# Kernel tuning notes

Hardware: AMD Instinct MI355X
Metric: run time of the kernel (lower is better)

The kernel has to match this reference:

```python
import jax, jax.numpy as jnp
import numpy as np

N1 = 4096
N2 = 4096


def _encoder(x, w1, b1, w2, b2, w3, b3):
    # fc1 -> fc2 -> fc3 -> relu (relu only after fc3, matching the torch code)
    h = x @ w1.T + b1
    h = h @ w2.T + b2
    h = h @ w3.T + b3
    return jax.nn.relu(h)


def _self_attention(x, adj, alpha, W):
    # tmp_i = sum_j [adj_ij==1] * alpha_ij * W * x_j ; tmp_i /= deg_i ; tmp_i += x_i (only if deg_i != 0)
    a = (adj == 1).astype(x.dtype)          # [N, N]
    deg = a.sum(axis=1)                     # [N]
    agg = (a * alpha) @ x                   # [N, 64] masked weighted aggregation
    agg = agg * W[0, 0]
    safe_deg = jnp.maximum(deg, 1.0)
    out = agg / safe_deg[:, None] + x       # residual
    return jnp.where((deg != 0.0)[:, None], out, jnp.zeros_like(out))


def setup_inputs() -> dict:
    key = jax.random.key(0)
    ks = jax.random.split(key, 20)
    s = 0.02  # weight scale to keep activations sane through the 4096->256->128->64 MLP
    inp = {
        "x1": jax.random.normal(ks[0], (N1, N1), jnp.float32),
        "x2": jax.random.normal(ks[1], (N2, N2), jnp.float32),
        "adj1": jax.random.randint(ks[2], (N1, N1), 0, 2, jnp.int32),
        "adj2": jax.random.randint(ks[3], (N2, N2), 0, 2, jnp.int32),
        "e1_w1": jax.random.normal(ks[4], (256, N1), jnp.float32) * s,
        "e1_b1": jnp.zeros((256,), jnp.float32),
        "e1_w2": jax.random.normal(ks[5], (128, 256), jnp.float32) * s,
        "e1_b2": jnp.zeros((128,), jnp.float32),
        "e1_w3": jax.random.normal(ks[6], (64, 128), jnp.float32) * s,
        "e1_b3": jnp.zeros((64,), jnp.float32),
        "e2_w1": jax.random.normal(ks[7], (256, N2), jnp.float32) * s,
        "e2_b1": jnp.zeros((256,), jnp.float32),
        "e2_w2": jax.random.normal(ks[8], (128, 256), jnp.float32) * s,
        "e2_b2": jnp.zeros((128,), jnp.float32),
        "e2_w3": jax.random.normal(ks[9], (64, 128), jnp.float32) * s,
        "e2_b3": jnp.zeros((64,), jnp.float32),
        "W": jax.random.normal(ks[10], (1, 1), jnp.float32),
        "alpha1": jax.random.normal(ks[11], (N1, N1), jnp.float32),
        "clf_w": jax.random.normal(ks[12], (2, (N1 + N2) * 64), jnp.float32) * s,
        "clf_b": jnp.zeros((2,), jnp.float32),
    }
    return inp


def reference(x1, x2, adj1, adj2,
              e1_w1, e1_b1, e1_w2, e1_b2, e1_w3, e1_b3,
              e2_w1, e2_b1, e2_w2, e2_b2, e2_w3, e2_b3,
              W, alpha1, clf_w, clf_b):
    h1 = _encoder(x1, e1_w1, e1_b1, e1_w2, e1_b2, e1_w3, e1_b3)  # [N1, 64]
    h2 = _encoder(x2, e2_w1, e2_b1, e2_w2, e2_b2, e2_w3, e2_b3)  # [N2, 64]
    # NOTE: original torch code uses self.alpha1 for BOTH graphs (alpha2 is unused)
    new1 = _self_attention(h1, adj1, alpha1, W)
    new2 = _self_attention(h2, adj2, alpha1[:N2, :N2], W)
    feat = jnp.concatenate([new1, new2], axis=0).reshape(1, -1)  # [1, (N1+N2)*64]
    return feat @ clf_w.T + clf_b  # [1, 2]
```

## Files before the change

kernel.cpp:

```cpp
#include <hip/hip_runtime.h>
#include <hip/hip_bf16.h>
#include <stdint.h>

#define N 4096

typedef __attribute__((ext_vector_type(4))) float f32x4;
typedef __attribute__((ext_vector_type(8))) short s16x8;

__device__ inline unsigned short f2bf(float f) {
    unsigned int u = __float_as_uint(f);
    u += 0x7fffu + ((u >> 16) & 1u);
    return (unsigned short)(u >> 16);
}
__device__ inline float bf2f(unsigned short h) {
    return __uint_as_float(((unsigned int)h) << 16);
}

__global__ void k0a(const float* __restrict__ w2a, const float* __restrict__ w3a,
                    const float* __restrict__ b1a, const float* __restrict__ b2a, const float* __restrict__ b3a,
                    const float* __restrict__ w2b, const float* __restrict__ w3b,
                    const float* __restrict__ b1b, const float* __restrict__ b2b, const float* __restrict__ b3b,
                    float* __restrict__ T, float* __restrict__ beff) {
    const int g  = blockIdx.x >> 5;
    const int nb = blockIdx.x & 31;
    const float* w2 = g ? w2b : w2a;
    const float* w3 = g ? w3b : w3a;
    const int c  = threadIdx.x;
    const int n0 = nb * 2;
    float a0 = 0.f, a1 = 0.f;
#pragma unroll 8
    for (int r = 0; r < 128; ++r) {
        float w = w2[r * 256 + c];
        a0 += w3[n0 * 128 + r] * w;
        a1 += w3[n0 * 128 + 128 + r] * w;
    }
    float* Tg = T + g * 64 * 256;
    Tg[n0 * 256 + c]       = a0;
    Tg[(n0 + 1) * 256 + c] = a1;

    if (nb == 0) {
        __shared__ float ps[256];
        __shared__ float u[128];
        const float* b1 = g ? b1b : b1a;
        const float* b2 = g ? b2b : b2a;
        const float* b3 = g ? b3b : b3a;
        {
            const int r = threadIdx.x >> 1, half = threadIdx.x & 1;
            float s = 0.f;
#pragma unroll 8
            for (int cc = 0; cc < 128; ++cc) s += w2[r * 256 + half * 128 + cc] * b1[half * 128 + cc];
            ps[threadIdx.x] = s;
        }
        __syncthreads();
        if (threadIdx.x < 128)
            u[threadIdx.x] = ps[2 * threadIdx.x] + ps[2 * threadIdx.x + 1] + b2[threadIdx.x];
        __syncthreads();
        {
            const int n = threadIdx.x >> 2, qr = threadIdx.x & 3;
            float s = 0.f;
#pragma unroll
            for (int r = 0; r < 32; ++r) s += w3[n * 128 + qr * 32 + r] * u[qr * 32 + r];
            ps[threadIdx.x] = s;
        }
        __syncthreads();
        if (threadIdx.x < 64)
            beff[g * 64 + threadIdx.x] = ps[4 * threadIdx.x] + ps[4 * threadIdx.x + 1]
                                       + ps[4 * threadIdx.x + 2] + ps[4 * threadIdx.x + 3] + b3[threadIdx.x];
    }
}

__global__ __launch_bounds__(256) void k0b(const float* __restrict__ w1a, const float* __restrict__ w1b,
                                           const float* __restrict__ T,
                                           unsigned short* __restrict__ Wfrag) {
    const int b  = blockIdx.x;
    const int g = b >> 8, n4 = (b >> 4) & 15, kchunk = b & 15;
    const float* w1 = g ? w1b : w1a;
    const int kx = kchunk * 256 + threadIdx.x;
    const float* Tg = T + (size_t)(g * 64 + n4 * 4) * 256;
    float acc[4] = {0.f, 0.f, 0.f, 0.f};
#pragma unroll 8
    for (int r = 0; r < 256; ++r) {
        float w = w1[(size_t)r * N + kx];
#pragma unroll
        for (int j = 0; j < 4; ++j) acc[j] += Tg[j * 256 + r] * w;
    }
    const int kc = kx >> 6, cc = (kx >> 5) & 1, q = (kx >> 3) & 3, ko = kx & 7;
#pragma unroll
    for (int j = 0; j < 4; ++j) {
        const int n = n4 * 4 + j;
        const int ng = n >> 4, l15 = n & 15;
        const int lane = q * 16 + l15;
        const unsigned short hi = f2bf(acc[j]);
        const unsigned short lo = f2bf(acc[j] - bf2f(hi));
        const size_t unit = ((((size_t)g * 64 + kc) * 4 + ng) * 2 + cc) * 2;
        Wfrag[unit * 512 + lane * 8 + ko]       = hi;
        Wfrag[(unit + 1) * 512 + lane * 8 + ko] = lo;
    }
}

__global__ __launch_bounds__(512, 4) void k1(const float* __restrict__ x1, const float* __restrict__ x2,
                                             const unsigned short* __restrict__ Wfrag,
                                             const float* __restrict__ beff,
                                             float* __restrict__ hf, unsigned short* __restrict__ hfrag) {
    const int b  = blockIdx.x;
    const int g  = b & 1;
    const int i0 = (b >> 1) * 16;
    const float* x = g ? x2 : x1;

    const int t = threadIdx.x;
    const int lane = t & 63, kg = t >> 6;
    const int q = lane >> 4, l15 = lane & 15;

    __shared__ float accs[8][4][64][4];
    __shared__ unsigned short htile[64][16];

    f32x4 acc[4];
#pragma unroll
    for (int ng = 0; ng < 4; ++ng) acc[ng] = (f32x4){0.f, 0.f, 0.f, 0.f};

    const float* xrow = x + (size_t)(i0 + l15) * N;
    for (int kk = 0; kk < 8; ++kk) {
        const int kc = kg * 8 + kk;
#pragma unroll
        for (int c = 0; c < 2; ++c) {
            const int ka = kc * 64 + c * 32 + q * 8;
            float4 a0 = *(const float4*)&xrow[ka];
            float4 a1 = *(const float4*)&xrow[ka + 4];
            s16x8 bh[4], bl[4];
#pragma unroll
            for (int ng = 0; ng < 4; ++ng) {
                const size_t unit = ((((size_t)g * 64 + kc) * 4 + ng) * 2 + c) * 2;
                bh[ng] = *(const s16x8*)&Wfrag[unit * 512 + lane * 8];
                bl[ng] = *(const s16x8*)&Wfrag[(unit + 1) * 512 + lane * 8];
            }
            float xv[8] = {a0.x, a0.y, a0.z, a0.w, a1.x, a1.y, a1.z, a1.w};
            s16x8 ah, al;
#pragma unroll
            for (int j = 0; j < 8; ++j) {
                unsigned short h = f2bf(xv[j]);
                ah[j] = (short)h;
                al[j] = (short)f2bf(xv[j] - bf2f(h));
            }
#pragma unroll
            for (int ng = 0; ng < 4; ++ng) {
                acc[ng] = __builtin_amdgcn_mfma_f32_16x16x32_bf16(al, bh[ng], acc[ng], 0, 0, 0);
                acc[ng] = __builtin_amdgcn_mfma_f32_16x16x32_bf16(ah, bl[ng], acc[ng], 0, 0, 0);
                acc[ng] = __builtin_amdgcn_mfma_f32_16x16x32_bf16(ah, bh[ng], acc[ng], 0, 0, 0);
            }
        }
    }
#pragma unroll
    for (int ng = 0; ng < 4; ++ng)
#pragma unroll
        for (int r = 0; r < 4; ++r) accs[kg][ng][lane][r] = acc[ng][r];
    __syncthreads();

    {
        const int ng = kg & 3, rh = kg >> 2;
        const int n = ng * 16 + l15;
        const float be = beff[g * 64 + n];
#pragma unroll
        for (int rr = 0; rr < 2; ++rr) {
            const int r = rh * 2 + rr;
            float s = 0.f;
#pragma unroll
            for (int k8 = 0; k8 < 8; ++k8) s += accs[k8][ng][lane][r];
            float v = fmaxf(s + be, 0.f);
            const int il = q * 4 + r;
            hf[(size_t)(g * N + i0 + il) * 64 + n] = v;
            htile[n][il] = f2bf(v);
        }
    }
    __syncthreads();

    if (t < 128) {
        const int ng2 = t >> 5, jh = (t >> 4) & 1, l = t & 15;
        uint4 v = *(const uint4*)&htile[ng2 * 16 + l][jh * 8];
        const int jc = i0 >> 6, c = (i0 >> 5) & 1, q0 = (i0 >> 3) & 3;
        const size_t unit = (((size_t)g * 4 + ng2) * 64 + jc) * 2 + c;
        *(uint4*)&hfrag[unit * 512 + (size_t)(q0 + jh) * 128 + l * 8] = v;
    }
}

__global__ __launch_bounds__(512, 2) void k2(const int* __restrict__ adj1, const int* __restrict__ adj2,
                                             const float* __restrict__ alpha,
                                             const unsigned short* __restrict__ hfrag,
                                             float* __restrict__ pagg, float* __restrict__ pdeg) {
    const int b  = blockIdx.x;
    const int ks = (b >> 1) & 3;
    const int i0 = ((((b >> 3) << 1) | (b & 1))) << 4;
    const int t = threadIdx.x;
    const int lane = t & 63, kg = t >> 6;
    const int q = lane >> 4, l15 = lane & 15;

    __shared__ __align__(16) unsigned short am[2][2][16][256];
    __shared__ float degp[2][16][32];
    float (*accs)[4][64][4] = reinterpret_cast<float (*)[4][64][4]>(&am[0][0][0][0]);

    f32x4 acc1[4], acc2[4];
#pragma unroll
    for (int ng = 0; ng < 4; ++ng) {
        acc1[ng] = (f32x4){0.f, 0.f, 0.f, 0.f};
        acc2[ng] = (f32x4){0.f, 0.f, 0.f, 0.f};
    }
    int deg1 = 0, deg2 = 0;

    const int srow = t >> 5, scg = t & 31;
    const size_t sbase = (size_t)(i0 + srow) * N + (size_t)ks * 1024 + (size_t)scg * 8;
    char* const amb = (char*)&am[0][0][0][0];
    const int swoff = (srow * 512 + scg * 16) ^ ((srow & 7) << 4);
    const int rdoff = (l15 * 512 + kg * 64 + q * 16) ^ ((l15 & 7) << 4);

    float4 sa0, sa1; int4 sj10, sj11, sj20, sj21;

#define K2_ISSUE(S) do { \
        const float* ap = alpha + sbase + (S) * 256; \
        sa0 = *(const float4*)ap; sa1 = *(const float4*)(ap + 4); \
        const int* p1 = adj1 + sbase + (S) * 256; \
        sj10 = *(const int4*)p1; sj11 = *(const int4*)(p1 + 4); \
        const int* p2 = adj2 + sbase + (S) * 256; \
        sj20 = *(const int4*)p2; sj21 = *(const int4*)(p2 + 4); \
    } while (0)

#define K2_CONVSTORE(BUF) do { \
        float av[8] = {sa0.x, sa0.y, sa0.z, sa0.w, sa1.x, sa1.y, sa1.z, sa1.w}; \
        int m1[8] = {sj10.x == 1, sj10.y == 1, sj10.z == 1, sj10.w == 1, \
                     sj11.x == 1, sj11.y == 1, sj11.z == 1, sj11.w == 1}; \
        int m2[8] = {sj20.x == 1, sj20.y == 1, sj20.z == 1, sj20.w == 1, \
                     sj21.x == 1, sj21.y == 1, sj21.z == 1, sj21.w == 1}; \
        s16x8 w1v, w2v; \
        _Pragma("unroll") \
        for (int j = 0; j < 8; ++j) { \
            unsigned short bv = f2bf(av[j]); \
            w1v[j] = m1[j] ? (short)bv : (short)0; \
            w2v[j] = m2[j] ? (short)bv : (short)0; \
            deg1 += m1[j]; deg2 += m2[j]; \
        } \
        *(s16x8*)(amb + (BUF) * 16384 + swoff) = w1v; \
        *(s16x8*)(amb + (BUF) * 16384 + 8192 + swoff) = w2v; \
    } while (0)

#define K2_COMPUTE(S) do { \
        const int jc = ks * 16 + (S) * 4 + (kg >> 1), cph = kg & 1; \
        s16x8 ha1[4], ha2[4]; \
        _Pragma("unroll") \
        for (int ng = 0; ng < 4; ++ng) { \
            const size_t u1 = (((size_t)ng) * 64 + jc) * 2 + cph; \
            const size_t u2 = (((size_t)(4 + ng)) * 64 + jc) * 2 + cph; \
            ha1[ng] = *(const s16x8*)&hfrag[u1 * 512 + lane * 8]; \
            ha2[ng] = *(const s16x8*)&hfrag[u2 * 512 + lane * 8]; \
        } \
        s16x8 bfa = *(const s16x8*)(amb + ((S) & 1) * 16384 + rdoff); \
        s16x8 bfb = *(const s16x8*)(amb + ((S) & 1) * 16384 + 8192 + rdoff); \
        _Pragma("unroll") \
        for (int ng = 0; ng < 4; ++ng) { \
            acc1[ng] = __builtin_amdgcn_mfma_f32_16x16x32_bf16(ha1[ng], bfa, acc1[ng], 0, 0, 0); \
            acc2[ng] = __builtin_amdgcn_mfma_f32_16x16x32_bf16(ha2[ng], bfb, acc2[ng], 0, 0, 0); \
        } \
    } while (0)

    K2_ISSUE(0);
    K2_CONVSTORE(0);
    __syncthreads();
#pragma unroll
    for (int s = 0; s < 4; ++s) {
        if (s < 3) K2_ISSUE(s + 1);
        K2_COMPUTE(s);
        if (s < 3) K2_CONVSTORE((s + 1) & 1);
        __syncthreads();
    }

    degp[0][srow][scg] = (float)deg1;
    degp[1][srow][scg] = (float)deg2;
#pragma unroll
    for (int ng = 0; ng < 4; ++ng)
#pragma unroll
        for (int r = 0; r < 4; ++r) accs[kg][ng][lane][r] = acc1[ng][r];
    __syncthreads();
    if (t < 32) {
        const int gg = t >> 4, row = t & 15;
        float s = 0.f;
#pragma unroll
        for (int c2 = 0; c2 < 32; ++c2) s += degp[gg][row][c2];
        pdeg[(size_t)(gg * 4 + ks) * 4096 + i0 + row] = s;
    }

    {
        const int ng = kg & 3, rh = kg >> 2;
        const int i = i0 + l15;
#pragma unroll
        for (int rr = 0; rr < 2; ++rr) {
            const int r = rh * 2 + rr;
            float s = 0.f;
#pragma unroll
            for (int k8 = 0; k8 < 8; ++k8) s += accs[k8][ng][lane][r];
            const int n = ng * 16 + q * 4 + r;
            pagg[(((size_t)ks * 4096 + i) << 6) + n] = s;
        }
    }
    __syncthreads();
#pragma unroll
    for (int ng = 0; ng < 4; ++ng)
#pragma unroll
        for (int r = 0; r < 4; ++r) accs[kg][ng][lane][r] = acc2[ng][r];
    __syncthreads();
    {
        const int ng = kg & 3, rh = kg >> 2;
        const int i = i0 + l15;
#pragma unroll
        for (int rr = 0; rr < 2; ++rr) {
            const int r = rh * 2 + rr;
            float s = 0.f;
#pragma unroll
            for (int k8 = 0; k8 < 8; ++k8) s += accs[k8][ng][lane][r];
            const int n = ng * 16 + q * 4 + r;
            pagg[(((size_t)(4 + ks) * 4096 + i) << 6) + n] = s;
        }
    }
#undef K2_ISSUE
#undef K2_CONVSTORE
#undef K2_COMPUTE
}

__global__ __launch_bounds__(256) void k2b(const float* __restrict__ pagg, const float* __restrict__ pdeg,
                                           const float* __restrict__ hf, const float* __restrict__ Wp,
                                           float* __restrict__ outv) {
    const int idx = blockIdx.x * 256 + threadIdx.x;
    const int gi  = idx >> 4;
    const int nq  = idx & 15;
    const int g   = gi >> 12, i = gi & 4095;
    const float W00 = Wp[0];

    float dg = 0.f;
#pragma unroll
    for (int ks = 0; ks < 4; ++ks) dg += pdeg[(size_t)(g * 4 + ks) * 4096 + i];

    f32x4 s = (f32x4){0.f, 0.f, 0.f, 0.f};
#pragma unroll
    for (int ks = 0; ks < 4; ++ks) {
        const f32x4 p = *(const f32x4*)&pagg[(((size_t)(g * 4 + ks) * 4096 + i) << 6) + nq * 4];
        s += p;
    }
    const f32x4 hv = *(const f32x4*)&hf[((size_t)gi << 6) + nq * 4];
    const float dmax = fmaxf(dg, 1.f);
    f32x4 o;
#pragma unroll
    for (int j = 0; j < 4; ++j)
        o[j] = (dg != 0.f) ? (s[j] * W00 / dmax + hv[j]) : 0.f;
    *(f32x4*)&outv[((size_t)gi << 6) + nq * 4] = o;
}

__global__ __launch_bounds__(256) void k3a(const float* __restrict__ feat, const float* __restrict__ clfw,
                                           float* __restrict__ part) {
    const int t = threadIdx.x;
    const size_t idx = (size_t)blockIdx.x * 2048 + (size_t)t * 8;
    float4 a0 = *(const float4*)&feat[idx];
    float4 a1 = *(const float4*)&feat[idx + 4];
    float4 c0 = *(const float4*)&clfw[idx];
    float4 c1 = *(const float4*)&clfw[idx + 4];
    float4 d0 = *(const float4*)&clfw[524288 + idx];
    float4 d1 = *(const float4*)&clfw[524288 + idx + 4];
    float s0 = a0.x * c0.x + a0.y * c0.y + a0.z * c0.z + a0.w * c0.w
             + a1.x * c1.x + a1.y * c1.y + a1.z * c1.z + a1.w * c1.w;
    float s1 = a0.x * d0.x + a0.y * d0.y + a0.z * d0.z + a0.w * d0.w
             + a1.x * d1.x + a1.y * d1.y + a1.z * d1.z + a1.w * d1.w;
    __shared__ float r0[256], r1[256];
    r0[t] = s0; r1[t] = s1;
    __syncthreads();
    for (int s = 128; s > 0; s >>= 1) {
        if (t < s) { r0[t] += r0[t + s]; r1[t] += r1[t + s]; }
        __syncthreads();
    }
    if (t == 0) { part[blockIdx.x * 2] = r0[0]; part[blockIdx.x * 2 + 1] = r1[0]; }
}

__global__ void k3b(const float* __restrict__ part, const float* __restrict__ clfb,
                    float* __restrict__ outp) {
    const int t = threadIdx.x;
    __shared__ float r0[256], r1[256];
    r0[t] = part[t * 2]; r1[t] = part[t * 2 + 1];
    __syncthreads();
    for (int s = 128; s > 0; s >>= 1) {
        if (t < s) { r0[t] += r0[t + s]; r1[t] += r1[t + s]; }
        __syncthreads();
    }
    if (t == 0) { outp[0] = r0[0] + clfb[0]; outp[1] = r1[0] + clfb[1]; }
}

extern "C" void kernel_launch(void* const* d_in, const int* in_sizes, int n_in,
                              void* d_out, int out_size, void* d_ws, size_t ws_size,
                              hipStream_t stream) {
    const float* x1   = (const float*)d_in[0];
    const float* x2   = (const float*)d_in[1];
    const int*   adj1 = (const int*)d_in[2];
    const int*   adj2 = (const int*)d_in[3];
    const float* e1w1 = (const float*)d_in[4];
    const float* e1b1 = (const float*)d_in[5];
    const float* e1w2 = (const float*)d_in[6];
    const float* e1b2 = (const float*)d_in[7];
    const float* e1w3 = (const float*)d_in[8];
    const float* e1b3 = (const float*)d_in[9];
    const float* e2w1 = (const float*)d_in[10];
    const float* e2b1 = (const float*)d_in[11];
    const float* e2w2 = (const float*)d_in[12];
    const float* e2b2 = (const float*)d_in[13];
    const float* e2w3 = (const float*)d_in[14];
    const float* e2b3 = (const float*)d_in[15];
    const float* Wp   = (const float*)d_in[16];
    const float* alph = (const float*)d_in[17];
    const float* clfw = (const float*)d_in[18];
    const float* clfb = (const float*)d_in[19];

    char* wsb = (char*)d_ws;
    unsigned short* Wfrag = (unsigned short*)(wsb);
    float* newv = (float*)(wsb);
    unsigned short* hfrag = (unsigned short*)(wsb + (2u << 20));
    float* hf   = (float*)(wsb + (3u << 20));
    float* T    = (float*)(wsb + (5u << 20));
    float* beff = (float*)(wsb + (5u << 20) + (1u << 17));
    float* part = (float*)(wsb + (5u << 20) + (1u << 17) + 4096);
    float* pagg = (float*)(wsb + (6u << 20));
    float* pdeg = (float*)(wsb + (14u << 20));

    hipLaunchKernelGGL(k0a, dim3(64), dim3(256), 0, stream,
                       e1w2, e1w3, e1b1, e1b2, e1b3, e2w2, e2w3, e2b1, e2b2, e2b3, T, beff);
    hipLaunchKernelGGL(k0b, dim3(512), dim3(256), 0, stream, e1w1, e2w1, T, Wfrag);
    hipLaunchKernelGGL(k1, dim3(512), dim3(512), 0, stream, x1, x2, Wfrag, beff, hf, hfrag);
    hipLaunchKernelGGL(k2, dim3(1024), dim3(512), 0, stream, adj1, adj2, alph, hfrag, pagg, pdeg);
    hipLaunchKernelGGL(k2b, dim3(512), dim3(256), 0, stream, pagg, pdeg, hf, Wp, newv);
    hipLaunchKernelGGL(k3a, dim3(256), dim3(256), 0, stream, newv, clfw, part);
    hipLaunchKernelGGL(k3b, dim3(1), dim3(256), 0, stream, part, clfb, (float*)d_out);
}
```

Baseline: 395.0 us.

## Split k1 GEMM into 64-row tiles with split-K partials and separate reduce kernel

k1 now gives each block 64 rows and a quarter of K, so each Wfrag fragment loaded is reused across four row groups instead of one. Partial sums go to a workspace buffer, and a new k1b kernel sums them and applies bias and relu before writing hf and hfrag. The main loop is also unrolled with double-buffered register loads so the next x and W fragments are fetched while the MFMAs run. In exchange it adds an extra launch, a round trip of the partials through global memory, and higher register pressure (launch bounds lowered to 2 blocks).

```diff
diff --git a/kernel.cpp b/kernel.cpp
--- a/kernel.cpp
+++ b/kernel.cpp
@@ -98,79 +98,118 @@
     }
 }
 
-__global__ __launch_bounds__(512, 4) void k1(const float* __restrict__ x1, const float* __restrict__ x2,
+__global__ __launch_bounds__(512, 2) void k1(const float* __restrict__ x1, const float* __restrict__ x2,
                                              const unsigned short* __restrict__ Wfrag,
-                                             const float* __restrict__ beff,
-                                             float* __restrict__ hf, unsigned short* __restrict__ hfrag) {
+                                             float* __restrict__ ph) {
     const int b  = blockIdx.x;
-    const int g  = b & 1;
-    const int i0 = (b >> 1) * 16;
+    const int rt = b >> 2, ks = b & 3;
+    const int g  = rt >> 6;
+    const int rbase = (rt & 63) * 64;
     const float* x = g ? x2 : x1;
 
     const int t = threadIdx.x;
-    const int lane = t & 63, kg = t >> 6;
+    const int lane = t & 63, w = t >> 6;
+    const int rg = w & 3, kh = w >> 2;
     const int q = lane >> 4, l15 = lane & 15;
 
-    __shared__ float accs[8][4][64][4];
-    __shared__ unsigned short htile[64][16];
+    __shared__ float accs_h[4][4][64][4];
 
     f32x4 acc[4];
 #pragma unroll
     for (int ng = 0; ng < 4; ++ng) acc[ng] = (f32x4){0.f, 0.f, 0.f, 0.f};
 
-    const float* xrow = x + (size_t)(i0 + l15) * N;
-    for (int kk = 0; kk < 8; ++kk) {
-        const int kc = kg * 8 + kk;
-#pragma unroll
-        for (int c = 0; c < 2; ++c) {
-            const int ka = kc * 64 + c * 32 + q * 8;
-            float4 a0 = *(const float4*)&xrow[ka];
-            float4 a1 = *(const float4*)&xrow[ka + 4];
-            s16x8 bh[4], bl[4];
-#pragma unroll
-            for (int ng = 0; ng < 4; ++ng) {
-                const size_t unit = ((((size_t)g * 64 + kc) * 4 + ng) * 2 + c) * 2;
-                bh[ng] = *(const s16x8*)&Wfrag[unit * 512 + lane * 8];
-                bl[ng] = *(const s16x8*)&Wfrag[(unit + 1) * 512 + lane * 8];
-            }
-            float xv[8] = {a0.x, a0.y, a0.z, a0.w, a1.x, a1.y, a1.z, a1.w};
-            s16x8 ah, al;
-#pragma unroll
-            for (int j = 0; j < 8; ++j) {
-                unsigned short h = f2bf(xv[j]);
-                ah[j] = (short)h;
-                al[j] = (short)f2bf(xv[j] - bf2f(h));
-            }
-#pragma unroll
-            for (int ng = 0; ng < 4; ++ng) {
-                acc[ng] = __builtin_amdgcn_mfma_f32_16x16x32_bf16(al, bh[ng], acc[ng], 0, 0, 0);
-                acc[ng] = __builtin_amdgcn_mfma_f32_16x16x32_bf16(ah, bl[ng], acc[ng], 0, 0, 0);
-                acc[ng] = __builtin_amdgcn_mfma_f32_16x16x32_bf16(ah, bh[ng], acc[ng], 0, 0, 0);
+    const float* xrow = x + (size_t)(rbase + rg * 16 + l15) * N;
+    const int kcbase = ks * 16 + kh * 8;
+
+    float4 pa0, pa1, ra0, ra1;
+    s16x8 pbh[4], pbl[4], rbh[4], rbl[4];
+
+#define K1_LOAD(A0, A1, BH, BL, IT) do { \
+        const int kc_ = kcbase + ((IT) >> 1), c_ = (IT) & 1; \
+        const int ka_ = kc_ * 64 + c_ * 32 + q * 8; \
+        A0 = *(const float4*)&xrow[ka_]; \
+        A1 = *(const float4*)&xrow[ka_ + 4]; \
+        _Pragma("unroll") \
+        for (int ng = 0; ng < 4; ++ng) { \
+            const size_t unit = ((((size_t)g * 64 + kc_) * 4 + ng) * 2 + c_) * 2; \
+            BH[ng] = *(const s16x8*)&Wfrag[unit * 512 + lane * 8]; \
+            BL[ng] = *(const s16x8*)&Wfrag[(unit + 1) * 512 + lane * 8]; \
+        } \
+    } while (0)
+
+#define K1_COMP(A0, A1, BH, BL) do { \
+        float xv[8] = {A0.x, A0.y, A0.z, A0.w, A1.x, A1.y, A1.z, A1.w}; \
+        s16x8 ah, al; \
+        _Pragma("unroll") \
+        for (int j = 0; j < 8; ++j) { \
+            unsigned short hh = f2bf(xv[j]); \
+            ah[j] = (short)hh; \
+            al[j] = (short)f2bf(xv[j] - bf2f(hh)); \
+        } \
+        _Pragma("unroll") \
+        for (int ng = 0; ng < 4; ++ng) { \
+            acc[ng] = __builtin_amdgcn_mfma_f32_16x16x32_bf16(al, BH[ng], acc[ng], 0, 0, 0); \
+            acc[ng] = __builtin_amdgcn_mfma_f32_16x16x32_bf16(ah, BL[ng], acc[ng], 0, 0, 0); \
+            acc[ng] = __builtin_amdgcn_mfma_f32_16x16x32_bf16(ah, BH[ng], acc[ng], 0, 0, 0); \
+        } \
+    } while (0)
+
+    K1_LOAD(pa0, pa1, pbh, pbl, 0);
+#pragma unroll
+    for (int it2 = 0; it2 < 8; ++it2) {
+        K1_LOAD(ra0, ra1, rbh, rbl, 2 * it2 + 1);
+        K1_COMP(pa0, pa1, pbh, pbl);
+        if (it2 < 7) K1_LOAD(pa0, pa1, pbh, pbl, 2 * it2 + 2);
+        K1_COMP(ra0, ra1, rbh, rbl);
+    }
+#undef K1_LOAD
+#undef K1_COMP
+
+    if (kh == 1) {
+#pragma unroll
+        for (int ng = 0; ng < 4; ++ng)
+#pragma unroll
+            for (int r = 0; r < 4; ++r) accs_h[rg][ng][lane][r] = acc[ng][r];
+    }
+    __syncthreads();
+    if (kh == 0) {
+        const int girow = g * 4096 + rbase + rg * 16 + q * 4;
+#pragma unroll
+        for (int ng = 0; ng < 4; ++ng) {
+            const int n = ng * 16 + l15;
+#pragma unroll
+            for (int r = 0; r < 4; ++r) {
+                float s = acc[ng][r] + accs_h[rg][ng][lane][r];
+                ph[((size_t)ks * 8192 + girow + r) * 64 + n] = s;
             }
         }
     }
-#pragma unroll
-    for (int ng = 0; ng < 4; ++ng)
-#pragma unroll
-        for (int r = 0; r < 4; ++r) accs[kg][ng][lane][r] = acc[ng][r];
-    __syncthreads();
-
-    {
-        const int ng = kg & 3, rh = kg >> 2;
-        const int n = ng * 16 + l15;
-        const float be = beff[g * 64 + n];
-#pragma unroll
-        for (int rr = 0; rr < 2; ++rr) {
-            const int r = rh * 2 + rr;
-            float s = 0.f;
-#pragma unroll
-            for (int k8 = 0; k8 < 8; ++k8) s += accs[k8][ng][lane][r];
-            float v = fmaxf(s + be, 0.f);
-            const int il = q * 4 + r;
-            hf[(size_t)(g * N + i0 + il) * 64 + n] = v;
-            htile[n][il] = f2bf(v);
-        }
-    }
+}
+
+__global__ __launch_bounds__(256) void k1b(const float* __restrict__ ph, const float* __restrict__ beff,
+                                           float* __restrict__ hf, unsigned short* __restrict__ hfrag) {
+    const int b = blockIdx.x;
+    const int g = b & 1;
+    const int i0 = (b >> 1) * 16;
+    const int t = threadIdx.x;
+    const int il = t >> 4, nq = t & 15;
+    const int gi = g * 4096 + i0 + il;
+
+    __shared__ unsigned short htile[64][16];
+
+    f32x4 s = (f32x4){0.f, 0.f, 0.f, 0.f};
+#pragma unroll
+    for (int ks = 0; ks < 4; ++ks)
+        s += *(const f32x4*)&ph[((size_t)ks * 8192 + gi) * 64 + nq * 4];
+    f32x4 o;
+#pragma unroll
+    for (int j = 0; j < 4; ++j) {
+        const int n = nq * 4 + j;
+        float v = fmaxf(s[j] + beff[g * 64 + n], 0.f);
+        o[j] = v;
+        htile[n][il] = f2bf(v);
+    }
+    *(f32x4*)&hf[(size_t)gi * 64 + nq * 4] = o;
     __syncthreads();
 
     if (t < 128) {
@@ -420,12 +459,14 @@
     float* beff = (float*)(wsb + (5u << 20) + (1u << 17));
     float* part = (float*)(wsb + (5u << 20) + (1u << 17) + 4096);
     float* pagg = (float*)(wsb + (6u << 20));
+    float* ph   = (float*)(wsb + (6u << 20));
     float* pdeg = (float*)(wsb + (14u << 20));
 
     hipLaunchKernelGGL(k0a, dim3(64), dim3(256), 0, stream,
                        e1w2, e1w3, e1b1, e1b2, e1b3, e2w2, e2w3, e2b1, e2b2, e2b3, T, beff);
     hipLaunchKernelGGL(k0b, dim3(512), dim3(256), 0, stream, e1w1, e2w1, T, Wfrag);
-    hipLaunchKernelGGL(k1, dim3(512), dim3(512), 0, stream, x1, x2, Wfrag, beff, hf, hfrag);
+    hipLaunchKernelGGL(k1, dim3(512), dim3(512), 0, stream, x1, x2, Wfrag, ph);
+    hipLaunchKernelGGL(k1b, dim3(512), dim3(256), 0, stream, ph, beff, hf, hfrag);
     hipLaunchKernelGGL(k2, dim3(1024), dim3(512), 0, stream, adj1, adj2, alph, hfrag, pagg, pdeg);
     hipLaunchKernelGGL(k2b, dim3(512), dim3(256), 0, stream, pagg, pdeg, hf, Wp, newv);
     hipLaunchKernelGGL(k3a, dim3(256), dim3(256), 0, stream, newv, clfw, part);
```

New measurement: 393.5 us. About the same (-0.4%).
